# Optimization experiments

Measured on AMD Instinct MI355X. Metric: run time of the kernel, lower is better.

## Reference

```python
import jax, jax.numpy as jnp
import numpy as np
import math

HIDDEN = 256
NUM_LAYERS = 3
NUM_TAU = 4
DT = 0.05
TAU_MIN, TAU_MAX = 0.01, 10.0
IN_SIZE = 128
OUT_SIZE = 64
B, S = 64, 2048


def setup_inputs() -> dict:
    key = jax.random.key(0)
    ks = jax.random.split(key, 16)
    H = HIDDEN
    def xavier(k, shape):
        fan_in, fan_out = shape[1], shape[0]
        lim = math.sqrt(6.0 / (fan_in + fan_out))
        return jax.random.uniform(k, shape, jnp.float32, -lim, lim)
    def ortho(k, n):
        a = jax.random.normal(k, (n, n), jnp.float32)
        q, r = jnp.linalg.qr(a)
        return q * jnp.sign(jnp.diag(r))[None, :]
    x = jax.random.normal(ks[0], (B, S, IN_SIZE), jnp.float32)
    # complexity_net: Linear(in,64) -> ReLU -> Linear(64,1) -> Sigmoid
    cw1 = xavier(ks[1], (64, IN_SIZE)); cb1 = jnp.zeros((64,), jnp.float32)
    cw2 = xavier(ks[2], (1, 64)); cb2 = jnp.zeros((1,), jnp.float32)
    # input projection
    pw = xavier(ks[3], (H, IN_SIZE)); pb = jnp.zeros((H,), jnp.float32)
    # per-layer recurrent params (stacked over layers)
    W_rec = jnp.stack([ortho(jax.random.fold_in(ks[4], i), H) for i in range(NUM_LAYERS)])
    W_in = jnp.stack([xavier(jax.random.fold_in(ks[5], i), (H, H)) for i in range(NUM_LAYERS)])
    bias = jnp.zeros((NUM_LAYERS, H), jnp.float32)
    tau_bands = jnp.tile(jnp.logspace(math.log10(TAU_MIN), math.log10(TAU_MAX), NUM_TAU, dtype=jnp.float32)[None, :], (NUM_LAYERS, 1))
    # tau_mixer: Linear(1, NUM_TAU) per layer -> weight [NUM_TAU,1] stored as [NUM_TAU]
    tmw = jax.random.uniform(ks[6], (NUM_LAYERS, NUM_TAU), jnp.float32, -1.0, 1.0)
    tmb = jax.random.uniform(ks[7], (NUM_LAYERS, NUM_TAU), jnp.float32, -1.0, 1.0)
    # output projection
    ow = xavier(ks[8], (OUT_SIZE, H)); ob = jnp.zeros((OUT_SIZE,), jnp.float32)
    return {"x": x, "cw1": cw1, "cb1": cb1, "cw2": cw2, "cb2": cb2,
            "pw": pw, "pb": pb, "W_rec": W_rec, "W_in": W_in, "bias": bias,
            "tau_bands": tau_bands, "tmw": tmw, "tmb": tmb, "ow": ow, "ob": ob}


def reference(x, cw1, cb1, cw2, cb2, pw, pb, W_rec, W_in, bias, tau_bands, tmw, tmb, ow, ob):
    # complexity net on time-mean of inputs -> [B, 1]
    comp = jax.nn.sigmoid(jax.nn.relu(x.mean(axis=1) @ cw1.T + cb1) @ cw2.T + cb2)
    h_seq = x @ pw.T + pb  # [B, S, H]
    hidden = jnp.zeros((x.shape[0], HIDDEN), x.dtype)
    for i in range(NUM_LAYERS):
        # tau_mixer: comp [B,1] * weight [NUM_TAU] -> logits [B, NUM_TAU]
        w = jax.nn.softmax(comp * tmw[i] + tmb[i], axis=-1)
        mixed_tau = jnp.sum(tau_bands[i] * w, axis=-1)          # [B]
        alpha = jnp.exp(-DT / mixed_tau)[:, None]               # [B,1] broadcast over H
        Wr, Wi, b = W_rec[i], W_in[i], bias[i]
        ext = h_seq @ Wi.T + b                                  # precompute input drive [B,S,H]
        def step(h, xt):
            act = jnp.tanh(h @ Wr.T + xt)
            h_new = alpha * h + (1.0 - alpha) * act
            return h_new, h_new
        hidden, outs = jax.lax.scan(step, hidden, ext.transpose(1, 0, 2))
        h_seq = outs.transpose(1, 0, 2)                         # [B,S,H]
    out = h_seq @ ow.T + ob                                     # [B,S,out]
    return out[:, -1]                                           # [B,out]
```

## Files before the change

kernel.cpp:

```cpp
#include <hip/hip_runtime.h>
#include <hip/hip_bf16.h>
#include <math.h>
#include <type_traits>

#define HIDDEN 256
#define SEQ 2048
#define BATCH 64
#define INSZ 128
#define OUTSZ 64
#define DTC 0.05f
#define CCH 32
#define CHS (SEQ / CCH)
#define TBLK (CHS / 32)

typedef _Float16 f16x8 __attribute__((ext_vector_type(8)));
typedef float f32x4 __attribute__((ext_vector_type(4)));

__global__ __launch_bounds__(1024) void prep_kernel(
    const float* __restrict__ x, const float* __restrict__ cw1, const float* __restrict__ cb1,
    const float* __restrict__ cw2, const float* __restrict__ cb2,
    const float* __restrict__ tau_b, const float* __restrict__ tmw, const float* __restrict__ tmb,
    float* __restrict__ alphas, float* __restrict__ h_carry)
{
    __shared__ float p_lds[8][128];
    __shared__ float xm[128];
    __shared__ float t1[64];
    int b = blockIdx.x;
    int tid = threadIdx.x;
    if (tid < 256) {
        h_carry[0 * 16384 + b * 256 + tid] = 0.f;
        h_carry[1 * 16384 + b * 256 + tid] = 0.f;
        h_carry[2 * 16384 + b * 256 + tid] = 0.f;
    }
    int c = tid & 127, sh = tid >> 7;
    const float* xb = x + (size_t)b * SEQ * INSZ;
    float s = 0.f;
    for (int t = sh * 256; t < (sh + 1) * 256; ++t) s += xb[(size_t)t * INSZ + c];
    p_lds[sh][c] = s;
    __syncthreads();
    if (tid < 128) {
        float m = 0.f;
        #pragma unroll
        for (int i = 0; i < 8; ++i) m += p_lds[i][tid];
        xm[tid] = m / (float)SEQ;
    }
    __syncthreads();
    if (tid < 64) {
        float acc = cb1[tid];
        for (int k = 0; k < 128; ++k) acc += xm[k] * cw1[tid * 128 + k];
        t1[tid] = fmaxf(acc, 0.f);
    }
    __syncthreads();
    if (tid == 0) {
        float acc = cb2[0];
        for (int k = 0; k < 64; ++k) acc += t1[k] * cw2[k];
        float comp = 1.f / (1.f + expf(-acc));
        for (int i = 0; i < 3; ++i) {
            float lg[4], mx = -1e30f;
            for (int j = 0; j < 4; ++j) { lg[j] = comp * tmw[i * 4 + j] + tmb[i * 4 + j]; mx = fmaxf(mx, lg[j]); }
            float den = 0.f;
            for (int j = 0; j < 4; ++j) { lg[j] = expf(lg[j] - mx); den += lg[j]; }
            float mt = 0.f;
            for (int j = 0; j < 4; ++j) mt += tau_b[i * 4 + j] * (lg[j] / den);
            alphas[i * 64 + b] = expf(-DTC / mt);
        }
    }
}

__global__ __launch_bounds__(128) void wf_kernel(
    const float* __restrict__ W_in0, const float* __restrict__ pw,
    const float* __restrict__ pb, const float* __restrict__ bias0,
    float* __restrict__ Wf, float* __restrict__ bf)
{
    __shared__ float wrow[256];
    int j = blockIdx.x, k = threadIdx.x;
    for (int m = k; m < 256; m += 128) wrow[m] = W_in0[j * 256 + m];
    __syncthreads();
    float s = 0.f;
    for (int m = 0; m < 256; ++m) s = fmaf(wrow[m], pw[m * 128 + k], s);
    Wf[j * 128 + k] = s;
    if (k == 0) {
        float sb = bias0[j];
        for (int m = 0; m < 256; ++m) sb = fmaf(wrow[m], pb[m], sb);
        bf[j] = sb;
    }
}

__device__ __forceinline__ unsigned pkrtz(float a, float b) {
    return __builtin_bit_cast(unsigned, __builtin_amdgcn_cvt_pkrtz(a, b));
}

__global__ __launch_bounds__(64) void wpack_kernel(
    const float* __restrict__ W, _Float16* __restrict__ P)
{
    int blk = blockIdx.x;
    int wave = blk >> 5, mt = (blk >> 3) & 3, kt = blk & 7;
    int lane = threadIdx.x;
    int row = wave * 64 + mt * 16 + (lane & 15);
    int kcol = kt * 32 + (lane >> 4) * 8;
    const float4* s = (const float4*)(W + (size_t)row * 256 + kcol);
    float4 a = s[0], b = s[1];
    uint4 u = { pkrtz(a.x, a.y), pkrtz(a.z, a.w), pkrtz(b.x, b.y), pkrtz(b.z, b.w) };
    *(uint4*)((char*)P + (size_t)blk * 1024 + lane * 16) = u;
}

__device__ __forceinline__ float fast_tanh(float x) {
    float ex = __expf(2.f * x);
    float r = __builtin_amdgcn_rcpf(ex + 1.f);
    return 1.f - 2.f * r;
}

__device__ __forceinline__ void barrier_lds_only() {
    asm volatile("s_waitcnt lgkmcnt(0)\n\ts_barrier" ::: "memory");
}

__global__ __launch_bounds__(256, 2) void gemm0_kernel(
    const float* __restrict__ Asrc,
    const float* __restrict__ W,
    const float* __restrict__ bias,
    float* __restrict__ C)
{
    constexpr int KD = 128, KT = 4, ROWB = 256;
    __shared__ alignas(16) char alds[32 * ROWB];
    const int tid = threadIdx.x;
    const int wave = tid >> 6, lane = tid & 63;
    const int bl = lane & 15, q = lane >> 4;
    const int m0 = blockIdx.x * 32;

    f16x8 bfrag[4][KT];
    float bv[4];
    #pragma unroll
    for (int nt = 0; nt < 4; ++nt) {
        int n = wave * 64 + nt * 16 + bl;
        const float* wr = W + (size_t)n * KD;
        #pragma unroll
        for (int kt = 0; kt < KT; ++kt) {
            const float4* wp = (const float4*)(wr + kt * 32 + q * 8);
            float4 u0 = wp[0], u1 = wp[1];
            uint4 u = { pkrtz(u0.x, u0.y), pkrtz(u0.z, u0.w),
                        pkrtz(u1.x, u1.y), pkrtz(u1.z, u1.w) };
            bfrag[nt][kt] = __builtin_bit_cast(f16x8, u);
        }
        bv[nt] = bias[n];
    }
    #pragma unroll
    for (int it = 0; it < 2; ++it) {
        int idx = tid + it * 256;
        int row = idx >> 4, chunk = idx & 15;
        const float4* sp = (const float4*)(Asrc + (size_t)(m0 + row) * KD + chunk * 8);
        float4 f0 = sp[0], f1 = sp[1];
        uint4 u = { pkrtz(f0.x, f0.y), pkrtz(f0.z, f0.w),
                    pkrtz(f1.x, f1.y), pkrtz(f1.z, f1.w) };
        *(uint4*)(alds + row * ROWB + ((chunk * 16) ^ ((row & 7) << 4))) = u;
    }
    __syncthreads();

    f32x4 acc[2][4];
    #pragma unroll
    for (int mt = 0; mt < 2; ++mt)
        #pragma unroll
        for (int nt = 0; nt < 4; ++nt) acc[mt][nt] = (f32x4){0.f, 0.f, 0.f, 0.f};
    #pragma unroll
    for (int kt = 0; kt < KT; ++kt) {
        int inner = kt * 64 + q * 16;
        f16x8 a0 = __builtin_bit_cast(f16x8,
            *(const uint4*)(alds + (0 * 16 + bl) * ROWB + (inner ^ ((bl & 7) << 4))));
        f16x8 a1 = __builtin_bit_cast(f16x8,
            *(const uint4*)(alds + (1 * 16 + bl) * ROWB + (inner ^ ((bl & 7) << 4))));
        #pragma unroll
        for (int nt = 0; nt < 4; ++nt) {
            acc[0][nt] = __builtin_amdgcn_mfma_f32_16x16x32_f16(a0, bfrag[nt][kt], acc[0][nt], 0, 0, 0);
            acc[1][nt] = __builtin_amdgcn_mfma_f32_16x16x32_f16(a1, bfrag[nt][kt], acc[1][nt], 0, 0, 0);
        }
    }
    #pragma unroll
    for (int mt = 0; mt < 2; ++mt)
        #pragma unroll
        for (int nt = 0; nt < 4; ++nt) {
            int col = wave * 64 + nt * 16 + bl;
            #pragma unroll
            for (int r = 0; r < 4; ++r)
                C[(size_t)(m0 + mt * 16 + q * 4 + r) * 256 + col] = acc[mt][nt][r] + bv[nt];
        }
}

__device__ __forceinline__ void scan_chunk(
    char* smem, float* buf, const _Float16* __restrict__ Wp,
    const float* __restrict__ alphas, float* __restrict__ h_carry,
    int b, int c, int write_all)
{
    _Float16 (*hlds)[256] = (_Float16 (*)[256])smem;
    const int tid = threadIdx.x;
    const int wave = tid >> 6, lane = tid & 63;
    const int bl = lane & 15, q = lane >> 4;
    const int mt_own = bl >> 2, r_own = bl & 3;
    const int m = wave * 64 + mt_own * 16 + q * 4 + r_own;

    f16x8 afrag[4][8];
    #pragma unroll
    for (int mt = 0; mt < 4; ++mt)
        #pragma unroll
        for (int kt = 0; kt < 8; ++kt)
            afrag[mt][kt] = __builtin_bit_cast(f16x8,
                *(const uint4*)((const char*)Wp + (size_t)(((wave * 4 + mt) * 8 + kt) * 64 + lane) * 16));

    const float alpha = alphas[b], onema = 1.f - alpha;
    float* bb = buf + (size_t)b * SEQ * HIDDEN;
    const int t0 = c * CHS, tend = t0 + CHS;

    float h_reg = h_carry[b * 256 + m];
    hlds[0][m] = (_Float16)h_reg;
    float e_cur = bb[(size_t)t0 * HIDDEN + m];
    float e_n1  = bb[(size_t)(t0 + 1) * HIDDEN + m];
    __syncthreads();

    auto step = [&](auto CB, int t) {
        constexpr int CUR = decltype(CB)::value;
        const char* rb = (const char*)&hlds[CUR][0];
        uint4 bq0 = *(const uint4*)(rb + q * 16);
        uint4 bq1 = *(const uint4*)(rb + 64 + q * 16);
        uint4 bq2 = *(const uint4*)(rb + 128 + q * 16);
        uint4 bq3 = *(const uint4*)(rb + 192 + q * 16);
        uint4 bq4 = *(const uint4*)(rb + 256 + q * 16);
        uint4 bq5 = *(const uint4*)(rb + 320 + q * 16);
        uint4 bq6 = *(const uint4*)(rb + 384 + q * 16);
        uint4 bq7 = *(const uint4*)(rb + 448 + q * 16);
        float e_n2 = 0.f;
        if (t + 2 < tend) e_n2 = bb[(size_t)(t + 2) * HIDDEN + m];

        f32x4 a0 = {0.f,0.f,0.f,0.f}, a1 = {0.f,0.f,0.f,0.f};
        f32x4 a2 = {0.f,0.f,0.f,0.f}, a3 = {0.f,0.f,0.f,0.f};
        #define MSTEP(BQ, KT) { f16x8 bf = __builtin_bit_cast(f16x8, BQ);                  \
            a0 = __builtin_amdgcn_mfma_f32_16x16x32_f16(afrag[0][KT], bf, a0, 0, 0, 0);    \
            a1 = __builtin_amdgcn_mfma_f32_16x16x32_f16(afrag[1][KT], bf, a1, 0, 0, 0);    \
            a2 = __builtin_amdgcn_mfma_f32_16x16x32_f16(afrag[2][KT], bf, a2, 0, 0, 0);    \
            a3 = __builtin_amdgcn_mfma_f32_16x16x32_f16(afrag[3][KT], bf, a3, 0, 0, 0); }
        MSTEP(bq0, 0) MSTEP(bq1, 1) MSTEP(bq2, 2) MSTEP(bq3, 3)
        MSTEP(bq4, 4) MSTEP(bq5, 5) MSTEP(bq6, 6) MSTEP(bq7, 7)
        #undef MSTEP

        f32x4 am = (mt_own == 0) ? a0 : (mt_own == 1) ? a1 : (mt_own == 2) ? a2 : a3;
        float s  = (r_own == 0) ? am[0] : (r_own == 1) ? am[1] : (r_own == 2) ? am[2] : am[3];

        float act = fast_tanh(s + e_cur);
        h_reg = alpha * h_reg + onema * act;
        hlds[CUR ^ 1][m] = (_Float16)h_reg;
        if (write_all)
            *((_Float16*)(bb + (size_t)t * HIDDEN) + m) = (_Float16)h_reg;
        barrier_lds_only();
        e_cur = e_n1;
        e_n1 = e_n2;
    };

    for (int t = t0; t < tend; t += 2) {
        step(std::integral_constant<int, 0>{}, t);
        step(std::integral_constant<int, 1>{}, t + 1);
    }
    h_carry[b * 256 + m] = h_reg;
}

__device__ __forceinline__ void gemm_chunk(
    char* smem, float* buf, const _Float16* __restrict__ Wp,
    const float* __restrict__ bias, int g, int c)
{
    constexpr int KT = 8, ROWB = 512;
    char* alds = smem;
    const int tid = threadIdx.x;
    const int wave = tid >> 6, lane = tid & 63;
    const int bl = lane & 15, q = lane >> 4;
    const size_t m0 = (size_t)(g / TBLK) * SEQ + (size_t)c * CHS + (g % TBLK) * 32;

    f16x8 bfrag[4][KT];
    float bv[4];
    #pragma unroll
    for (int nt = 0; nt < 4; ++nt) {
        #pragma unroll
        for (int kt = 0; kt < KT; ++kt)
            bfrag[nt][kt] = __builtin_bit_cast(f16x8,
                *(const uint4*)((const char*)Wp + (size_t)(((wave * 4 + nt) * 8 + kt) * 64 + lane) * 16));
        bv[nt] = bias[wave * 64 + nt * 16 + bl];
    }
    #pragma unroll
    for (int it = 0; it < 4; ++it) {
        int idx = tid + it * 256;
        int row = idx >> 5, chunk = idx & 31;
        uint4 u = *(const uint4*)((const char*)buf + (m0 + row) * 1024 + chunk * 16);
        *(uint4*)(alds + row * ROWB + ((chunk * 16) ^ ((row & 7) << 4))) = u;
    }
    __syncthreads();

    f32x4 acc[2][4];
    #pragma unroll
    for (int mt = 0; mt < 2; ++mt)
        #pragma unroll
        for (int nt = 0; nt < 4; ++nt) acc[mt][nt] = (f32x4){0.f, 0.f, 0.f, 0.f};
    #pragma unroll
    for (int kt = 0; kt < KT; ++kt) {
        int inner = kt * 64 + q * 16;
        f16x8 a0 = __builtin_bit_cast(f16x8,
            *(const uint4*)(alds + (0 * 16 + bl) * ROWB + (inner ^ ((bl & 7) << 4))));
        f16x8 a1 = __builtin_bit_cast(f16x8,
            *(const uint4*)(alds + (1 * 16 + bl) * ROWB + (inner ^ ((bl & 7) << 4))));
        #pragma unroll
        for (int nt = 0; nt < 4; ++nt) {
            acc[0][nt] = __builtin_amdgcn_mfma_f32_16x16x32_f16(a0, bfrag[nt][kt], acc[0][nt], 0, 0, 0);
            acc[1][nt] = __builtin_amdgcn_mfma_f32_16x16x32_f16(a1, bfrag[nt][kt], acc[1][nt], 0, 0, 0);
        }
    }
    #pragma unroll
    for (int mt = 0; mt < 2; ++mt)
        #pragma unroll
        for (int nt = 0; nt < 4; ++nt) {
            int col = wave * 64 + nt * 16 + bl;
            #pragma unroll
            for (int r = 0; r < 4; ++r)
                buf[(m0 + mt * 16 + q * 4 + r) * 256 + col] = acc[mt][nt][r] + bv[nt];
        }
}

__global__ __launch_bounds__(256, 1) void stage_kernel(
    int stage, float* buf,
    const _Float16* __restrict__ wpk,
    const float* __restrict__ bias,  const float* __restrict__ alphas,
    float* __restrict__ h_carry)
{
    __shared__ alignas(16) char smem[16384];
    int blk = blockIdx.x;
    if (blk < 192) {
        int layer = blk >> 6;
        int c = stage - 2 * layer;
        if (c < 0 || c >= CCH) return;
        scan_chunk(smem, buf, wpk + (size_t)layer * 65536, alphas + layer * 64,
                   h_carry + (size_t)layer * 16384, blk & 63, c, layer < 2);
    } else {
        int g = blk - 192;
        int which = g / (64 * TBLK);
        int gl = g % (64 * TBLK);
        int c = stage - 1 - 2 * which;
        if (c < 0 || c >= CCH) return;
        gemm_chunk(smem, buf, wpk + (size_t)(3 + which) * 65536, bias + (which + 1) * 256, gl, c);
    }
}

__global__ __launch_bounds__(256) void outproj_kernel(
    const float* __restrict__ h_carry, const float* __restrict__ ow, const float* __restrict__ ob,
    float* __restrict__ out)
{
    __shared__ float h_l[256];
    __shared__ float p_lds[4][64];
    int b = blockIdx.x;
    int tid = threadIdx.x;
    h_l[tid] = h_carry[b * 256 + tid];
    __syncthreads();
    int o = tid & 63, qq = tid >> 6;
    float s = 0.f;
    const float4* wp = (const float4*)(ow + o * 256 + qq * 64);
    const float4* hp = (const float4*)(h_l + qq * 64);
    #pragma unroll
    for (int m = 0; m < 16; ++m) {
        float4 wv = wp[m]; float4 hv = hp[m];
        s = fmaf(wv.x, hv.x, s); s = fmaf(wv.y, hv.y, s);
        s = fmaf(wv.z, hv.z, s); s = fmaf(wv.w, hv.w, s);
    }
    p_lds[qq][o] = s;
    __syncthreads();
    if (tid < 64)
        out[b * 64 + tid] = p_lds[0][tid] + p_lds[1][tid] + p_lds[2][tid] + p_lds[3][tid] + ob[tid];
}

extern "C" void kernel_launch(void* const* d_in, const int* in_sizes, int n_in,
                              void* d_out, int out_size, void* d_ws, size_t ws_size,
                              hipStream_t stream)
{
    const float* x     = (const float*)d_in[0];
    const float* cw1   = (const float*)d_in[1];
    const float* cb1   = (const float*)d_in[2];
    const float* cw2   = (const float*)d_in[3];
    const float* cb2   = (const float*)d_in[4];
    const float* pw    = (const float*)d_in[5];
    const float* pb    = (const float*)d_in[6];
    const float* W_rec = (const float*)d_in[7];
    const float* W_in  = (const float*)d_in[8];
    const float* bias  = (const float*)d_in[9];
    const float* tau_b = (const float*)d_in[10];
    const float* tmw   = (const float*)d_in[11];
    const float* tmb   = (const float*)d_in[12];
    const float* ow    = (const float*)d_in[13];
    const float* ob    = (const float*)d_in[14];
    float* out = (float*)d_out;

    char* ws = (char*)d_ws;
    float*     alphas  = (float*)ws;
    float*     h_carry = (float*)(ws + 1024);
    float*     bf      = (float*)(ws + 197632);
    float*     Wf      = (float*)(ws + 198656);
    _Float16*  wpk     = (_Float16*)(ws + 329728);
    float*     buf     = (float*)(ws + 1048576);

    const int MROWS = BATCH * SEQ;
    const int NGBLK = 192 + 2 * 64 * TBLK;

    prep_kernel<<<64, 1024, 0, stream>>>(x, cw1, cb1, cw2, cb2, tau_b, tmw, tmb, alphas, h_carry);
    wf_kernel<<<256, 128, 0, stream>>>(W_in, pw, pb, bias, Wf, bf);

    wpack_kernel<<<128, 64, 0, stream>>>(W_rec,                wpk);
    wpack_kernel<<<128, 64, 0, stream>>>(W_rec + 65536,        wpk + 65536);
    wpack_kernel<<<128, 64, 0, stream>>>(W_rec + 131072,       wpk + 2 * 65536);
    wpack_kernel<<<128, 64, 0, stream>>>(W_in + 65536,         wpk + 3 * 65536);
    wpack_kernel<<<128, 64, 0, stream>>>(W_in + 131072,        wpk + 4 * 65536);

    gemm0_kernel<<<MROWS / 32, 256, 0, stream>>>(x, Wf, bf, buf);

    for (int s = 0; s < CCH + 4; ++s)
        stage_kernel<<<NGBLK, 256, 0, stream>>>(s, buf, wpk, bias, alphas, h_carry);

    outproj_kernel<<<64, 256, 0, stream>>>(h_carry + 2 * 16384, ow, ob, out);
}
```

Baseline: 1.494 ms.

## Fuse next-layer input projection into recurrent scan and pipeline layer-0 GEMM per chunk

Each scan block now also multiplies its freshly computed hidden state by the next layer's input weights and writes that layer's drive directly, so the separate per-chunk GEMM blocks are gone. The layer-0 input GEMM moves into the staged launch loop as per-chunk blocks, and the stage count drops because layers are offset by one stage instead of two. This removes the extra round-trip of hidden states through memory and the standalone GEMM launch. In exchange, the serial scan steps do twice the MFMA work and hold twice the weight registers, which could lengthen the critical recurrent path.

```diff
diff --git a/kernel.cpp b/kernel.cpp
--- a/kernel.cpp
+++ b/kernel.cpp
@@ -11,7 +11,6 @@
 #define DTC 0.05f
 #define CCH 32
 #define CHS (SEQ / CCH)
-#define TBLK (CHS / 32)
 
 typedef _Float16 f16x8 __attribute__((ext_vector_type(8)));
 typedef float f32x4 __attribute__((ext_vector_type(4)));
@@ -114,80 +113,14 @@
     asm volatile("s_waitcnt lgkmcnt(0)\n\ts_barrier" ::: "memory");
 }
 
-__global__ __launch_bounds__(256, 2) void gemm0_kernel(
-    const float* __restrict__ Asrc,
-    const float* __restrict__ W,
-    const float* __restrict__ bias,
-    float* __restrict__ C)
-{
-    constexpr int KD = 128, KT = 4, ROWB = 256;
-    __shared__ alignas(16) char alds[32 * ROWB];
-    const int tid = threadIdx.x;
-    const int wave = tid >> 6, lane = tid & 63;
-    const int bl = lane & 15, q = lane >> 4;
-    const int m0 = blockIdx.x * 32;
-
-    f16x8 bfrag[4][KT];
-    float bv[4];
-    #pragma unroll
-    for (int nt = 0; nt < 4; ++nt) {
-        int n = wave * 64 + nt * 16 + bl;
-        const float* wr = W + (size_t)n * KD;
-        #pragma unroll
-        for (int kt = 0; kt < KT; ++kt) {
-            const float4* wp = (const float4*)(wr + kt * 32 + q * 8);
-            float4 u0 = wp[0], u1 = wp[1];
-            uint4 u = { pkrtz(u0.x, u0.y), pkrtz(u0.z, u0.w),
-                        pkrtz(u1.x, u1.y), pkrtz(u1.z, u1.w) };
-            bfrag[nt][kt] = __builtin_bit_cast(f16x8, u);
-        }
-        bv[nt] = bias[n];
-    }
-    #pragma unroll
-    for (int it = 0; it < 2; ++it) {
-        int idx = tid + it * 256;
-        int row = idx >> 4, chunk = idx & 15;
-        const float4* sp = (const float4*)(Asrc + (size_t)(m0 + row) * KD + chunk * 8);
-        float4 f0 = sp[0], f1 = sp[1];
-        uint4 u = { pkrtz(f0.x, f0.y), pkrtz(f0.z, f0.w),
-                    pkrtz(f1.x, f1.y), pkrtz(f1.z, f1.w) };
-        *(uint4*)(alds + row * ROWB + ((chunk * 16) ^ ((row & 7) << 4))) = u;
-    }
-    __syncthreads();
-
-    f32x4 acc[2][4];
-    #pragma unroll
-    for (int mt = 0; mt < 2; ++mt)
-        #pragma unroll
-        for (int nt = 0; nt < 4; ++nt) acc[mt][nt] = (f32x4){0.f, 0.f, 0.f, 0.f};
-    #pragma unroll
-    for (int kt = 0; kt < KT; ++kt) {
-        int inner = kt * 64 + q * 16;
-        f16x8 a0 = __builtin_bit_cast(f16x8,
-            *(const uint4*)(alds + (0 * 16 + bl) * ROWB + (inner ^ ((bl & 7) << 4))));
-        f16x8 a1 = __builtin_bit_cast(f16x8,
-            *(const uint4*)(alds + (1 * 16 + bl) * ROWB + (inner ^ ((bl & 7) << 4))));
-        #pragma unroll
-        for (int nt = 0; nt < 4; ++nt) {
-            acc[0][nt] = __builtin_amdgcn_mfma_f32_16x16x32_f16(a0, bfrag[nt][kt], acc[0][nt], 0, 0, 0);
-            acc[1][nt] = __builtin_amdgcn_mfma_f32_16x16x32_f16(a1, bfrag[nt][kt], acc[1][nt], 0, 0, 0);
-        }
-    }
-    #pragma unroll
-    for (int mt = 0; mt < 2; ++mt)
-        #pragma unroll
-        for (int nt = 0; nt < 4; ++nt) {
-            int col = wave * 64 + nt * 16 + bl;
-            #pragma unroll
-            for (int r = 0; r < 4; ++r)
-                C[(size_t)(m0 + mt * 16 + q * 4 + r) * 256 + col] = acc[mt][nt][r] + bv[nt];
-        }
-}
-
-__device__ __forceinline__ void scan_chunk(
-    char* smem, float* buf, const _Float16* __restrict__ Wp,
+template<bool FUSE>
+__device__ __forceinline__ void scan_chunk_f(
+    char* smem, float* buf,
+    const _Float16* __restrict__ Wp,
+    const _Float16* __restrict__ Wn,
+    const float* __restrict__ bias_n,
     const float* __restrict__ alphas, float* __restrict__ h_carry,
-    int b, int c, int write_all)
+    int b, int c)
 {
     _Float16 (*hlds)[256] = (_Float16 (*)[256])smem;
     const int tid = threadIdx.x;
@@ -203,6 +136,16 @@
         for (int kt = 0; kt < 8; ++kt)
             afrag[mt][kt] = __builtin_bit_cast(f16x8,
                 *(const uint4*)((const char*)Wp + (size_t)(((wave * 4 + mt) * 8 + kt) * 64 + lane) * 16));
+    f16x8 wfrag[4][8];
+    if (FUSE) {
+        #pragma unroll
+        for (int mt = 0; mt < 4; ++mt)
+            #pragma unroll
+            for (int kt = 0; kt < 8; ++kt)
+                wfrag[mt][kt] = __builtin_bit_cast(f16x8,
+                    *(const uint4*)((const char*)Wn + (size_t)(((wave * 4 + mt) * 8 + kt) * 64 + lane) * 16));
+    }
+    const float bn = FUSE ? bias_n[m] : 0.f;
 
     const float alpha = alphas[b], onema = 1.f - alpha;
     float* bb = buf + (size_t)b * SEQ * HIDDEN;
@@ -230,23 +173,36 @@
 
         f32x4 a0 = {0.f,0.f,0.f,0.f}, a1 = {0.f,0.f,0.f,0.f};
         f32x4 a2 = {0.f,0.f,0.f,0.f}, a3 = {0.f,0.f,0.f,0.f};
-        #define MSTEP(BQ, KT) { f16x8 bf = __builtin_bit_cast(f16x8, BQ);                  \
-            a0 = __builtin_amdgcn_mfma_f32_16x16x32_f16(afrag[0][KT], bf, a0, 0, 0, 0);    \
-            a1 = __builtin_amdgcn_mfma_f32_16x16x32_f16(afrag[1][KT], bf, a1, 0, 0, 0);    \
-            a2 = __builtin_amdgcn_mfma_f32_16x16x32_f16(afrag[2][KT], bf, a2, 0, 0, 0);    \
-            a3 = __builtin_amdgcn_mfma_f32_16x16x32_f16(afrag[3][KT], bf, a3, 0, 0, 0); }
-        MSTEP(bq0, 0) MSTEP(bq1, 1) MSTEP(bq2, 2) MSTEP(bq3, 3)
-        MSTEP(bq4, 4) MSTEP(bq5, 5) MSTEP(bq6, 6) MSTEP(bq7, 7)
-        #undef MSTEP
+        #define MSTEP(FR, BQ, KT, X0, X1, X2, X3) { f16x8 bf_ = __builtin_bit_cast(f16x8, BQ); \
+            X0 = __builtin_amdgcn_mfma_f32_16x16x32_f16(FR[0][KT], bf_, X0, 0, 0, 0);          \
+            X1 = __builtin_amdgcn_mfma_f32_16x16x32_f16(FR[1][KT], bf_, X1, 0, 0, 0);          \
+            X2 = __builtin_amdgcn_mfma_f32_16x16x32_f16(FR[2][KT], bf_, X2, 0, 0, 0);          \
+            X3 = __builtin_amdgcn_mfma_f32_16x16x32_f16(FR[3][KT], bf_, X3, 0, 0, 0); }
+        MSTEP(afrag, bq0, 0, a0, a1, a2, a3) MSTEP(afrag, bq1, 1, a0, a1, a2, a3)
+        MSTEP(afrag, bq2, 2, a0, a1, a2, a3) MSTEP(afrag, bq3, 3, a0, a1, a2, a3)
+        MSTEP(afrag, bq4, 4, a0, a1, a2, a3) MSTEP(afrag, bq5, 5, a0, a1, a2, a3)
+        MSTEP(afrag, bq6, 6, a0, a1, a2, a3) MSTEP(afrag, bq7, 7, a0, a1, a2, a3)
+
+        if (FUSE) {
+            f32x4 e0 = {0.f,0.f,0.f,0.f}, e1 = {0.f,0.f,0.f,0.f};
+            f32x4 e2 = {0.f,0.f,0.f,0.f}, e3 = {0.f,0.f,0.f,0.f};
+            MSTEP(wfrag, bq0, 0, e0, e1, e2, e3) MSTEP(wfrag, bq1, 1, e0, e1, e2, e3)
+            MSTEP(wfrag, bq2, 2, e0, e1, e2, e3) MSTEP(wfrag, bq3, 3, e0, e1, e2, e3)
+            MSTEP(wfrag, bq4, 4, e0, e1, e2, e3) MSTEP(wfrag, bq5, 5, e0, e1, e2, e3)
+            MSTEP(wfrag, bq6, 6, e0, e1, e2, e3) MSTEP(wfrag, bq7, 7, e0, e1, e2, e3)
+            if (t > t0) {
+                f32x4 em = (mt_own == 0) ? e0 : (mt_own == 1) ? e1 : (mt_own == 2) ? e2 : e3;
+                float ev = (r_own == 0) ? em[0] : (r_own == 1) ? em[1] : (r_own == 2) ? em[2] : em[3];
+                bb[(size_t)(t - 1) * HIDDEN + m] = ev + bn;
+            }
+        }
 
         f32x4 am = (mt_own == 0) ? a0 : (mt_own == 1) ? a1 : (mt_own == 2) ? a2 : a3;
-        float s  = (r_own == 0) ? am[0] : (r_own == 1) ? am[1] : (r_own == 2) ? am[2] : am[3];
-
-        float act = fast_tanh(s + e_cur);
+        float sv = (r_own == 0) ? am[0] : (r_own == 1) ? am[1] : (r_own == 2) ? am[2] : am[3];
+
+        float act = fast_tanh(sv + e_cur);
         h_reg = alpha * h_reg + onema * act;
         hlds[CUR ^ 1][m] = (_Float16)h_reg;
-        if (write_all)
-            *((_Float16*)(bb + (size_t)t * HIDDEN) + m) = (_Float16)h_reg;
         barrier_lds_only();
         e_cur = e_n1;
         e_n1 = e_n2;
@@ -256,89 +212,133 @@
         step(std::integral_constant<int, 0>{}, t);
         step(std::integral_constant<int, 1>{}, t + 1);
     }
+
+    if (FUSE) {
+        const char* rb = (const char*)&hlds[0][0];
+        uint4 bq0 = *(const uint4*)(rb + q * 16);
+        uint4 bq1 = *(const uint4*)(rb + 64 + q * 16);
+        uint4 bq2 = *(const uint4*)(rb + 128 + q * 16);
+        uint4 bq3 = *(const uint4*)(rb + 192 + q * 16);
+        uint4 bq4 = *(const uint4*)(rb + 256 + q * 16);
+        uint4 bq5 = *(const uint4*)(rb + 320 + q * 16);
+        uint4 bq6 = *(const uint4*)(rb + 384 + q * 16);
+        uint4 bq7 = *(const uint4*)(rb + 448 + q * 16);
+        f32x4 e0 = {0.f,0.f,0.f,0.f}, e1 = {0.f,0.f,0.f,0.f};
+        f32x4 e2 = {0.f,0.f,0.f,0.f}, e3 = {0.f,0.f,0.f,0.f};
+        MSTEP(wfrag, bq0, 0, e0, e1, e2, e3) MSTEP(wfrag, bq1, 1, e0, e1, e2, e3)
+        MSTEP(wfrag, bq2, 2, e0, e1, e2, e3) MSTEP(wfrag, bq3, 3, e0, e1, e2, e3)
+        MSTEP(wfrag, bq4, 4, e0, e1, e2, e3) MSTEP(wfrag, bq5, 5, e0, e1, e2, e3)
+        MSTEP(wfrag, bq6, 6, e0, e1, e2, e3) MSTEP(wfrag, bq7, 7, e0, e1, e2, e3)
+        f32x4 em = (mt_own == 0) ? e0 : (mt_own == 1) ? e1 : (mt_own == 2) ? e2 : e3;
+        float ev = (r_own == 0) ? em[0] : (r_own == 1) ? em[1] : (r_own == 2) ? em[2] : em[3];
+        bb[(size_t)(tend - 1) * HIDDEN + m] = ev + bn;
+        #undef MSTEP
+    }
     h_carry[b * 256 + m] = h_reg;
 }
 
-__device__ __forceinline__ void gemm_chunk(
-    char* smem, float* buf, const _Float16* __restrict__ Wp,
-    const float* __restrict__ bias, int g, int c)
-{
-    constexpr int KT = 8, ROWB = 512;
+__device__ __forceinline__ void gemm0_chunk(
+    char* smem, const float* __restrict__ x, const float* __restrict__ Wf,
+    const float* __restrict__ bf, float* __restrict__ buf, int gl, int c)
+{
+    constexpr int KD = 128, KT = 4, ROWB = 256;
     char* alds = smem;
     const int tid = threadIdx.x;
     const int wave = tid >> 6, lane = tid & 63;
     const int bl = lane & 15, q = lane >> 4;
-    const size_t m0 = (size_t)(g / TBLK) * SEQ + (size_t)c * CHS + (g % TBLK) * 32;
 
     f16x8 bfrag[4][KT];
     float bv[4];
     #pragma unroll
     for (int nt = 0; nt < 4; ++nt) {
-        #pragma unroll
-        for (int kt = 0; kt < KT; ++kt)
-            bfrag[nt][kt] = __builtin_bit_cast(f16x8,
-                *(const uint4*)((const char*)Wp + (size_t)(((wave * 4 + nt) * 8 + kt) * 64 + lane) * 16));
-        bv[nt] = bias[wave * 64 + nt * 16 + bl];
-    }
-    #pragma unroll
-    for (int it = 0; it < 4; ++it) {
-        int idx = tid + it * 256;
-        int row = idx >> 5, chunk = idx & 31;
-        uint4 u = *(const uint4*)((const char*)buf + (m0 + row) * 1024 + chunk * 16);
-        *(uint4*)(alds + row * ROWB + ((chunk * 16) ^ ((row & 7) << 4))) = u;
-    }
-    __syncthreads();
-
-    f32x4 acc[2][4];
-    #pragma unroll
-    for (int mt = 0; mt < 2; ++mt)
-        #pragma unroll
-        for (int nt = 0; nt < 4; ++nt) acc[mt][nt] = (f32x4){0.f, 0.f, 0.f, 0.f};
-    #pragma unroll
-    for (int kt = 0; kt < KT; ++kt) {
-        int inner = kt * 64 + q * 16;
-        f16x8 a0 = __builtin_bit_cast(f16x8,
-            *(const uint4*)(alds + (0 * 16 + bl) * ROWB + (inner ^ ((bl & 7) << 4))));
-        f16x8 a1 = __builtin_bit_cast(f16x8,
-            *(const uint4*)(alds + (1 * 16 + bl) * ROWB + (inner ^ ((bl & 7) << 4))));
-        #pragma unroll
-        for (int nt = 0; nt < 4; ++nt) {
-            acc[0][nt] = __builtin_amdgcn_mfma_f32_16x16x32_f16(a0, bfrag[nt][kt], acc[0][nt], 0, 0, 0);
-            acc[1][nt] = __builtin_amdgcn_mfma_f32_16x16x32_f16(a1, bfrag[nt][kt], acc[1][nt], 0, 0, 0);
+        int n = wave * 64 + nt * 16 + bl;
+        const float* wr = Wf + (size_t)n * KD;
+        #pragma unroll
+        for (int kt = 0; kt < KT; ++kt) {
+            const float4* wp = (const float4*)(wr + kt * 32 + q * 8);
+            float4 u0 = wp[0], u1 = wp[1];
+            uint4 u = { pkrtz(u0.x, u0.y), pkrtz(u0.z, u0.w),
+                        pkrtz(u1.x, u1.y), pkrtz(u1.z, u1.w) };
+            bfrag[nt][kt] = __builtin_bit_cast(f16x8, u);
         }
-    }
-    #pragma unroll
-    for (int mt = 0; mt < 2; ++mt)
-        #pragma unroll
-        for (int nt = 0; nt < 4; ++nt) {
-            int col = wave * 64 + nt * 16 + bl;
+        bv[nt] = bf[n];
+    }
+
+    for (int half = 0; half < 2; ++half) {
+        size_t m0 = (size_t)gl * SEQ + (size_t)c * CHS + (size_t)half * 32;
+        const float* Asrc = x + m0 * KD;
+
+        __syncthreads();
+        #pragma unroll
+        for (int it = 0; it < 2; ++it) {
+            int idx = tid + it * 256;
+            int row = idx >> 4, chunk = idx & 15;
+            const float4* sp = (const float4*)(Asrc + (size_t)row * KD + chunk * 8);
+            float4 f0 = sp[0], f1 = sp[1];
+            uint4 u = { pkrtz(f0.x, f0.y), pkrtz(f0.z, f0.w),
+                        pkrtz(f1.x, f1.y), pkrtz(f1.z, f1.w) };
+            *(uint4*)(alds + row * ROWB + ((chunk * 16) ^ ((row & 7) << 4))) = u;
+        }
+        __syncthreads();
+
+        f32x4 acc[2][4];
+        #pragma unroll
+        for (int mt = 0; mt < 2; ++mt)
             #pragma unroll
-            for (int r = 0; r < 4; ++r)
-                buf[(m0 + mt * 16 + q * 4 + r) * 256 + col] = acc[mt][nt][r] + bv[nt];
+            for (int nt = 0; nt < 4; ++nt) acc[mt][nt] = (f32x4){0.f, 0.f, 0.f, 0.f};
+        #pragma unroll
+        for (int kt = 0; kt < KT; ++kt) {
+            int inner = kt * 64 + q * 16;
+            f16x8 a0 = __builtin_bit_cast(f16x8,
+                *(const uint4*)(alds + (0 * 16 + bl) * ROWB + (inner ^ ((bl & 7) << 4))));
+            f16x8 a1 = __builtin_bit_cast(f16x8,
+                *(const uint4*)(alds + (1 * 16 + bl) * ROWB + (inner ^ ((bl & 7) << 4))));
+            #pragma unroll
+            for (int nt = 0; nt < 4; ++nt) {
+                acc[0][nt] = __builtin_amdgcn_mfma_f32_16x16x32_f16(a0, bfrag[nt][kt], acc[0][nt], 0, 0, 0);
+                acc[1][nt] = __builtin_amdgcn_mfma_f32_16x16x32_f16(a1, bfrag[nt][kt], acc[1][nt], 0, 0, 0);
+            }
         }
+        #pragma unroll
+        for (int mt = 0; mt < 2; ++mt)
+            #pragma unroll
+            for (int nt = 0; nt < 4; ++nt) {
+                int col = wave * 64 + nt * 16 + bl;
+                #pragma unroll
+                for (int r = 0; r < 4; ++r)
+                    buf[(m0 + mt * 16 + q * 4 + r) * 256 + col] = acc[mt][nt][r] + bv[nt];
+            }
+    }
 }
 
 __global__ __launch_bounds__(256, 1) void stage_kernel(
-    int stage, float* buf,
+    int stage, float* buf, const float* __restrict__ x,
     const _Float16* __restrict__ wpk,
-    const float* __restrict__ bias,  const float* __restrict__ alphas,
+    const float* __restrict__ Wf, const float* __restrict__ bf,
+    const float* __restrict__ bias, const float* __restrict__ alphas,
     float* __restrict__ h_carry)
 {
-    __shared__ alignas(16) char smem[16384];
+    __shared__ alignas(16) char smem[8192];
     int blk = blockIdx.x;
     if (blk < 192) {
         int layer = blk >> 6;
-        int c = stage - 2 * layer;
+        int c = stage - 1 - layer;
         if (c < 0 || c >= CCH) return;
-        scan_chunk(smem, buf, wpk + (size_t)layer * 65536, alphas + layer * 64,
-                   h_carry + (size_t)layer * 16384, blk & 63, c, layer < 2);
+        int b = blk & 63;
+        if (layer == 0)
+            scan_chunk_f<true>(smem, buf, wpk, wpk + 3 * 65536, bias + 256,
+                               alphas, h_carry, b, c);
+        else if (layer == 1)
+            scan_chunk_f<true>(smem, buf, wpk + 65536, wpk + 4 * 65536, bias + 512,
+                               alphas + 64, h_carry + 16384, b, c);
+        else
+            scan_chunk_f<false>(smem, buf, wpk + 2 * 65536, nullptr, nullptr,
+                                alphas + 128, h_carry + 2 * 16384, b, c);
     } else {
-        int g = blk - 192;
-        int which = g / (64 * TBLK);
-        int gl = g % (64 * TBLK);
-        int c = stage - 1 - 2 * which;
-        if (c < 0 || c >= CCH) return;
-        gemm_chunk(smem, buf, wpk + (size_t)(3 + which) * 65536, bias + (which + 1) * 256, gl, c);
+        int gl = blk - 192;
+        int c = stage;
+        if (c >= CCH) return;
+        gemm0_chunk(smem, x, Wf, bf, buf, gl, c);
     }
 }
 
@@ -397,22 +397,17 @@
     _Float16*  wpk     = (_Float16*)(ws + 329728);
     float*     buf     = (float*)(ws + 1048576);
 
-    const int MROWS = BATCH * SEQ;
-    const int NGBLK = 192 + 2 * 64 * TBLK;
-
     prep_kernel<<<64, 1024, 0, stream>>>(x, cw1, cb1, cw2, cb2, tau_b, tmw, tmb, alphas, h_carry);
     wf_kernel<<<256, 128, 0, stream>>>(W_in, pw, pb, bias, Wf, bf);
 
-    wpack_kernel<<<128, 64, 0, stream>>>(W_rec,                wpk);
-    wpack_kernel<<<128, 64, 0, stream>>>(W_rec + 65536,        wpk + 65536);
-    wpack_kernel<<<128, 64, 0, stream>>>(W_rec + 131072,       wpk + 2 * 65536);
-    wpack_kernel<<<128, 64, 0, stream>>>(W_in + 65536,         wpk + 3 * 65536);
-    wpack_kernel<<<128, 64, 0, stream>>>(W_in + 131072,        wpk + 4 * 65536);
-
-    gemm0_kernel<<<MROWS / 32, 256, 0, stream>>>(x, Wf, bf, buf);
-
-    for (int s = 0; s < CCH + 4; ++s)
-        stage_kernel<<<NGBLK, 256, 0, stream>>>(s, buf, wpk, bias, alphas, h_carry);
+    wpack_kernel<<<128, 64, 0, stream>>>(W_rec,          wpk);
+    wpack_kernel<<<128, 64, 0, stream>>>(W_rec + 65536,  wpk + 65536);
+    wpack_kernel<<<128, 64, 0, stream>>>(W_rec + 131072, wpk + 2 * 65536);
+    wpack_kernel<<<128, 64, 0, stream>>>(W_in + 65536,   wpk + 3 * 65536);
+    wpack_kernel<<<128, 64, 0, stream>>>(W_in + 131072,  wpk + 4 * 65536);
+
+    for (int s = 0; s < CCH + 3; ++s)
+        stage_kernel<<<256, 256, 0, stream>>>(s, buf, x, wpk, Wf, bf, bias, alphas, h_carry);
 
     outproj_kernel<<<64, 256, 0, stream>>>(h_carry + 2 * 16384, ow, ob, out);
 }
```

After: 2.209 ms. +47.8%, slower.
